# Kernel optimization log

Hardware: AMD Instinct MI355X
Metric: run time of the kernel (lower is better)

The kernel has to match this reference:

```python
import jax, jax.numpy as jnp
import numpy as np

B, N, IN, H, E = 8, 16383, 300, 512, 100  # complete binary tree, depth 14


def setup_inputs() -> dict:
    key = jax.random.key(0)
    ks = jax.random.split(key, 12)
    s = 0.05  # weight scale for numerical sanity
    return {
        "inputs": jax.random.normal(ks[0], (B, N, IN), jnp.float32),
        "edge_inputs": jax.random.normal(ks[1], (B, N, E), jnp.float32),
        "Wioux": jax.random.normal(ks[2], (3 * H, IN), jnp.float32) * s,
        "bioux": jax.random.normal(ks[3], (3 * H,), jnp.float32) * s,
        "Wiouh": jax.random.normal(ks[4], (3 * H, H), jnp.float32) * s,
        "biouh": jax.random.normal(ks[5], (3 * H,), jnp.float32) * s,
        "Wfx": jax.random.normal(ks[6], (H, IN), jnp.float32) * s,
        "bfx": jax.random.normal(ks[7], (H,), jnp.float32) * s,
        "Wfh": jax.random.normal(ks[8], (H, H), jnp.float32) * s,
        "bfh": jax.random.normal(ks[9], (H,), jnp.float32) * s,
        "We": jax.random.normal(ks[10], (H, E), jnp.float32) * s,
        "be": jax.random.normal(ks[11], (H,), jnp.float32) * s,
    }


def reference(inputs, edge_inputs, Wioux, bioux, Wiouh, biouh, Wfx, bfx, Wfh, bfh, We, be):
    # Level-batched TreeLSTM over a complete binary tree (BFS numbering:
    # children of node k are 2k+1, 2k+2). Same per-node math as the torch
    # recursion, with all nodes at a depth processed in one fused step.
    b, n_nodes, _ = inputs.shape
    hdim = Wiouh.shape[1]
    depth = int(np.log2(n_nodes + 1))
    h = jnp.zeros((b, n_nodes, hdim), inputs.dtype)
    c = jnp.zeros((b, n_nodes, hdim), inputs.dtype)
    for lvl in reversed(range(depth)):
        start = 2 ** lvl - 1
        n = 2 ** lvl
        x = inputs[:, start:start + n]                       # (B, n, IN)
        iou = jnp.einsum('bni,oi->bno', x, Wioux) + bioux + biouh
        if lvl == depth - 1:
            # leaves: child_c = child_h = 0, child_w = 0 => edge/f terms vanish
            fc_sum = jnp.zeros((b, n, hdim), inputs.dtype)
        else:
            cs = 2 * start + 1                               # first child index
            hc = h[:, cs:cs + 2 * n].reshape(b, n, 2, hdim)  # (B, n, 2, H)
            cc = c[:, cs:cs + 2 * n].reshape(b, n, 2, hdim)
            wc = edge_inputs[:, cs:cs + 2 * n].reshape(b, n, 2, -1)
            ex = jax.nn.sigmoid(jnp.einsum('bnke,he->bnkh', wc, We) + be)
            h_sum = (ex * hc).sum(axis=2)                    # edge-gated child sum
            iou = iou + jnp.einsum('bnh,oh->bno', h_sum, Wiouh)
            f = jax.nn.sigmoid(
                jnp.einsum('bnkh,oh->bnko', hc, Wfh) + bfh
                + (jnp.einsum('bni,hi->bnh', x, Wfx) + bfx)[:, :, None, :])
            fc_sum = (f * cc).sum(axis=2)
        i, o, u = jnp.split(iou, 3, axis=-1)
        c_lvl = jax.nn.sigmoid(i) * jnp.tanh(u) + fc_sum
        h_lvl = jax.nn.sigmoid(o) * jnp.tanh(c_lvl)
        c = c.at[:, start:start + n].set(c_lvl)
        h = h.at[:, start:start + n].set(h_lvl)
    # root state (c, h), concatenated along feature dim: (B, 2H)
    return jnp.concatenate([c[:, 0], h[:, 0]], axis=-1)
```

## Files before the change

kernel.cpp:

```cpp
#include <hip/hip_runtime.h>
#include <hip/hip_bf16.h>
#include <stdint.h>

#define B 8
#define NN 16383
#define INDIM 300
#define HDIM 512
#define EDIM 100

typedef short bf16x8 __attribute__((ext_vector_type(8)));
typedef float f32x4 __attribute__((ext_vector_type(4)));
typedef unsigned short ushort_t;

__device__ __forceinline__ float sigmoidf_(float v) { return 1.0f / (1.0f + __expf(-v)); }

__device__ __forceinline__ ushort_t f2b(float f) {
    union { float f; unsigned int u; } x; x.f = f;
    unsigned int u = x.u;
    return (ushort_t)((u + 0x7FFFu + ((u >> 16) & 1u)) >> 16);
}
__device__ __forceinline__ float b2f(ushort_t s) {
    union { float f; unsigned int u; } x; x.u = ((unsigned int)s) << 16; return x.f;
}
__device__ __forceinline__ bf16x8 zero8() {
    bf16x8 v;
#pragma unroll
    for (int i = 0; i < 8; ++i) v[i] = 0;
    return v;
}

__device__ __forceinline__ unsigned int pidx(int R, int col) {
    return (unsigned int)((R >> 4) * 8192 + (col >> 5) * 512 + ((col >> 3) & 3) * 128
                          + (R & 15) * 8 + (col & 7));
}

__device__ __forceinline__ size_t xlvl_base(int start) {
    return start ? (size_t)(start + 1) * 2560 : (size_t)0;
}

__global__ __launch_bounds__(256) void pack_kernel(
    const float* __restrict__ W, ushort_t* __restrict__ out,
    int Kdim, int Kt, int total)
{
    int idx = blockIdx.x * 256 + threadIdx.x;
    if (idx >= total) return;
    int lane = idx & 63;
    int kt = (idx >> 6) % Kt;
    int nt = idx / (Kt << 6);
    int n = nt * 16 + (lane & 15);
    int kb = kt * 32 + (lane >> 4) * 8;
    ushort_t v[8];
#pragma unroll
    for (int i = 0; i < 8; ++i) {
        int k = kb + i;
        v[i] = (k < Kdim) ? f2b(W[(size_t)n * Kdim + k]) : (ushort_t)0;
    }
    *reinterpret_cast<uint4*>(out + (size_t)idx * 8) = *reinterpret_cast<const uint4*>(v);
}

__global__ __launch_bounds__(256) void xpack_kernel(
    const float* __restrict__ inputs, ushort_t* __restrict__ xpk)
{
    int tid = blockIdx.x * 256 + threadIdx.x;
    if (tid >= NN * 8 * 40) return;
    int kr = tid & 3;
    int kt = (tid >> 2) % 10;
    int rb = tid / 40;
    int g = rb >> 3, b = rb & 7;
    int lvl = 31 - __clz(g + 1);
    int start = (1 << lvl) - 1;
    int R = (g - start) * 8 + b;
    int k0 = kt * 32 + kr * 8;
    ushort_t v[8];
#pragma unroll
    for (int i = 0; i < 8; i += 4) {
        int k = k0 + i;
        float4 xv = make_float4(0.f, 0.f, 0.f, 0.f);
        if (k + 4 <= INDIM)
            xv = *reinterpret_cast<const float4*>(&inputs[((size_t)b * NN + g) * INDIM + k]);
        v[i] = f2b(xv.x); v[i + 1] = f2b(xv.y); v[i + 2] = f2b(xv.z); v[i + 3] = f2b(xv.w);
    }
    size_t o = xlvl_base(start) + (size_t)(R >> 4) * 5120
             + (size_t)kt * 512 + (size_t)kr * 128 + (size_t)(R & 15) * 8;
    *reinterpret_cast<uint4*>(xpk + o) = *reinterpret_cast<const uint4*>(v);
}

__global__ __launch_bounds__(256) void children_kernel(
    const ushort_t* __restrict__ xpk, const float* __restrict__ edge_inputs,
    const ushort_t* __restrict__ pWfx, const float* __restrict__ bfx,
    const ushort_t* __restrict__ pWfh, const float* __restrict__ bfh,
    const ushort_t* __restrict__ pWe,  const float* __restrict__ be,
    const ushort_t* __restrict__ hX, const ushort_t* __restrict__ cX,
    ushort_t* __restrict__ hY, ushort_t* __restrict__ cY,
    int start, int n)
{
    const int nb = blockIdx.x * 4;
    const int pp = blockIdx.y;
    const int t = threadIdx.x;
    const int w = t >> 6, lane = t & 63;
    const int kr = lane >> 4, cl = lane & 15;

    __shared__ ushort_t wc[64][136];
    __shared__ ushort_t epi[64][264];

    for (int i = t; i < 64 * 32; i += 256) {
        int r = i >> 5, ch = i & 31;
        int kid = r >> 5, pr = r & 31, p = pr >> 3, b = pr & 7;
        int e = ch * 4;
        ushort_t vv[4] = {0, 0, 0, 0};
        if (e < EDIM && (nb + p) < n) {
            float4 xv = *reinterpret_cast<const float4*>(
                &edge_inputs[((size_t)b * NN + 2 * (start + nb + p) + 1 + kid) * EDIM + e]);
            vv[0] = f2b(xv.x); vv[1] = f2b(xv.y); vv[2] = f2b(xv.z); vv[3] = f2b(xv.w);
        }
        *reinterpret_cast<uint2*>(&wc[r][e]) = *reinterpret_cast<const uint2*>(vv);
    }
    __syncthreads();

    const bf16x8* fWfx = reinterpret_cast<const bf16x8*>(pWfx);
    const bf16x8* fWfh = reinterpret_cast<const bf16x8*>(pWfh);
    const bf16x8* fWe  = reinterpret_cast<const bf16x8*>(pWe);

    const ushort_t* xb = xpk + xlvl_base(start) + (size_t)(blockIdx.x * 2) * 5120 + (size_t)cl * 8;

    unsigned int cbase[4];
#pragma unroll
    for (int mt = 0; mt < 4; ++mt) {
        int kid = mt >> 1, mh = mt & 1;
        int p = 2 * mh + (cl >> 3);
        int b = cl & 7;
        cbase[mt] = ((nb + p) < n)
            ? (unsigned int)((nb + p) * 8192 + (kr * 16 + 8 * kid + b) * 8)
            : 0u;
    }

    const int ntb = w * 8 + pp * 4;

    f32x4 xfa[4][2];
#pragma unroll
    for (int q = 0; q < 4; ++q)
#pragma unroll
        for (int mh = 0; mh < 2; ++mh)
#pragma unroll
            for (int r = 0; r < 4; ++r) xfa[q][mh][r] = 0.f;
#pragma unroll 2
    for (int kt = 0; kt < 10; ++kt) {
        bf16x8 a0 = *reinterpret_cast<const bf16x8*>(xb + kt * 512 + kr * 128);
        bf16x8 a1 = *reinterpret_cast<const bf16x8*>(xb + 5120 + kt * 512 + kr * 128);
#pragma unroll
        for (int q = 0; q < 4; ++q) {
            bf16x8 bf_ = fWfx[(size_t)((ntb + q) * 10 + kt) * 64 + lane];
            xfa[q][0] = __builtin_amdgcn_mfma_f32_16x16x32_bf16(a0, bf_, xfa[q][0], 0, 0, 0);
            xfa[q][1] = __builtin_amdgcn_mfma_f32_16x16x32_bf16(a1, bf_, xfa[q][1], 0, 0, 0);
        }
    }
#pragma unroll
    for (int q = 0; q < 4; ++q) {
        float bv = bfx[(ntb + q) * 16 + cl];
#pragma unroll
        for (int mh = 0; mh < 2; ++mh)
#pragma unroll
            for (int r = 0; r < 4; ++r) xfa[q][mh][r] += bv;
    }

    {
        f32x4 eacc[4][4];
#pragma unroll
        for (int q = 0; q < 4; ++q)
#pragma unroll
            for (int mt = 0; mt < 4; ++mt)
#pragma unroll
                for (int r = 0; r < 4; ++r) eacc[q][mt][r] = 0.f;
#pragma unroll
        for (int kt = 0; kt < 4; ++kt) {
            bf16x8 av[4];
#pragma unroll
            for (int mt = 0; mt < 4; ++mt)
                av[mt] = *reinterpret_cast<const bf16x8*>(&wc[mt * 16 + cl][kt * 32 + kr * 8]);
#pragma unroll
            for (int q = 0; q < 4; ++q) {
                bf16x8 bf_ = fWe[(size_t)((ntb + q) * 4 + kt) * 64 + lane];
#pragma unroll
                for (int mt = 0; mt < 4; ++mt)
                    eacc[q][mt] = __builtin_amdgcn_mfma_f32_16x16x32_bf16(av[mt], bf_, eacc[q][mt], 0, 0, 0);
            }
        }
#pragma unroll
        for (int q = 0; q < 4; ++q) {
            float bev = be[(ntb + q) * 16 + cl];
#pragma unroll
            for (int mt = 0; mt < 4; ++mt)
#pragma unroll
                for (int r = 0; r < 4; ++r)
                    epi[mt * 16 + kr * 4 + r][(w * 4 + q) * 16 + cl] =
                        f2b(sigmoidf_(eacc[q][mt][r] + bev));
        }
    }
    __syncthreads();

#pragma unroll 1
    for (int it = 0; it < 4; ++it) {
        int task = it * 256 + t;
        int pb = task >> 5, cb = task & 31;
        int p = pb >> 3, b = pb & 7;
        if (nb + p < n) {
            int lc0 = cb * 8;
            int nt = ((cb >> 3) << 3) + pp * 4 + ((cb >> 1) & 3);
            int hh = cb & 1;
            int colc = (nt >> 1) * 512 + (((nt & 1) << 1) + hh) * 128;
            bf16x8 e0 = *reinterpret_cast<const bf16x8*>(&epi[pb][lc0]);
            bf16x8 e1 = *reinterpret_cast<const bf16x8*>(&epi[32 + pb][lc0]);
            const ushort_t* hb = hX + (unsigned int)((nb + p) * 8192 + colc + b * 8);
            bf16x8 h0 = *reinterpret_cast<const bf16x8*>(hb);
            bf16x8 h1 = *reinterpret_cast<const bf16x8*>(hb + 64);
            ushort_t res[8];
#pragma unroll
            for (int i = 0; i < 8; ++i)
                res[i] = f2b(b2f((ushort_t)e0[i]) * b2f((ushort_t)h0[i])
                           + b2f((ushort_t)e1[i]) * b2f((ushort_t)h1[i]));
            *reinterpret_cast<uint4*>(hY + (unsigned int)(((nb + p) >> 1) * 8192 + colc
                    + ((((nb + p) & 1) << 3) + b) * 8)) = *reinterpret_cast<const uint4*>(res);
        }
    }
    __syncthreads();

    {
        f32x4 facc[4][4];
#pragma unroll
        for (int q = 0; q < 4; ++q)
#pragma unroll
            for (int mt = 0; mt < 4; ++mt)
#pragma unroll
                for (int r = 0; r < 4; ++r) facc[q][mt][r] = 0.f;
#pragma unroll 4
        for (int kt = 0; kt < 16; ++kt) {
            bf16x8 av[4];
#pragma unroll
            for (int mt = 0; mt < 4; ++mt)
                av[mt] = *reinterpret_cast<const bf16x8*>(hX + cbase[mt] + kt * 512u);
#pragma unroll
            for (int q = 0; q < 4; ++q) {
                bf16x8 bf_ = fWfh[(size_t)((ntb + q) * 16 + kt) * 64 + lane];
#pragma unroll
                for (int mt = 0; mt < 4; ++mt)
                    facc[q][mt] = __builtin_amdgcn_mfma_f32_16x16x32_bf16(av[mt], bf_, facc[q][mt], 0, 0, 0);
            }
        }
#pragma unroll
        for (int q = 0; q < 4; ++q) {
            float bfhv = bfh[(ntb + q) * 16 + cl];
#pragma unroll
            for (int mt = 0; mt < 4; ++mt)
#pragma unroll
                for (int r = 0; r < 4; ++r)
                    epi[mt * 16 + kr * 4 + r][(w * 4 + q) * 16 + cl] =
                        f2b(sigmoidf_(facc[q][mt][r] + bfhv + xfa[q][mt & 1][r]));
        }
    }
    __syncthreads();

#pragma unroll 1
    for (int it = 0; it < 4; ++it) {
        int task = it * 256 + t;
        int pb = task >> 5, cb = task & 31;
        int p = pb >> 3, b = pb & 7;
        if (nb + p < n) {
            int lc0 = cb * 8;
            int nt = ((cb >> 3) << 3) + pp * 4 + ((cb >> 1) & 3);
            int hh = cb & 1;
            int colc = (nt >> 1) * 512 + (((nt & 1) << 1) + hh) * 128;
            bf16x8 f0 = *reinterpret_cast<const bf16x8*>(&epi[pb][lc0]);
            bf16x8 f1 = *reinterpret_cast<const bf16x8*>(&epi[32 + pb][lc0]);
            const ushort_t* cb_ = cX + (unsigned int)((nb + p) * 8192 + colc + b * 8);
            bf16x8 c0 = *reinterpret_cast<const bf16x8*>(cb_);
            bf16x8 c1 = *reinterpret_cast<const bf16x8*>(cb_ + 64);
            ushort_t res[8];
#pragma unroll
            for (int i = 0; i < 8; ++i)
                res[i] = f2b(b2f((ushort_t)f0[i]) * b2f((ushort_t)c0[i])
                           + b2f((ushort_t)f1[i]) * b2f((ushort_t)c1[i]));
            *reinterpret_cast<uint4*>(cY + (unsigned int)(((nb + p) >> 1) * 8192 + colc
                    + ((((nb + p) & 1) << 3) + b) * 8)) = *reinterpret_cast<const uint4*>(res);
        }
    }
}

template <bool LEAF, int JSPAN>
__global__ __launch_bounds__(256) void iou_kernel(
    const ushort_t* __restrict__ xpk,
    const ushort_t* __restrict__ pWioux, const float* __restrict__ bioux,
    const ushort_t* __restrict__ pWiouh, const float* __restrict__ biouh,
    const ushort_t* __restrict__ hYsum, const ushort_t* __restrict__ cYfc,
    ushort_t* __restrict__ hOut, ushort_t* __restrict__ cOut,
    int start, int n)
{
    const int nb = blockIdx.x * 8;
    const int t = threadIdx.x;
    const int w = t >> 6, lane = t & 63;
    const int kr = lane >> 4, cl = lane & 15;

    __shared__ ushort_t xsl[4 * 5120];
    __shared__ ushort_t p1[64][72];
    __shared__ ushort_t p2[64][72];

    {
        const ushort_t* xsrc = xpk + xlvl_base(start) + (size_t)(blockIdx.x * 4) * 5120;
        for (int i = t; i < 2560; i += 256)
            *reinterpret_cast<uint4*>(xsl + (size_t)i * 8) =
                *reinterpret_cast<const uint4*>(xsrc + (size_t)i * 8);
    }
    __syncthreads();

    const bf16x8* fWx = reinterpret_cast<const bf16x8*>(pWioux);
    const bf16x8* fWh = reinterpret_cast<const bf16x8*>(pWiouh);

    unsigned int hbase[4];
#pragma unroll
    for (int mt = 0; mt < 4; ++mt)
        hbase[mt] = (unsigned int)(((nb >> 1) + mt) * 8192 + lane * 8);

#pragma unroll 1
    for (int jj = 0; jj < JSPAN; ++jj) {
        const int j = blockIdx.y * JSPAN + jj;
        const int cnt = j * 4 + w;
        f32x4 acc[4][3];
#pragma unroll
        for (int mt = 0; mt < 4; ++mt)
#pragma unroll
            for (int q = 0; q < 3; ++q)
#pragma unroll
                for (int r = 0; r < 4; ++r) acc[mt][q][r] = 0.f;

#pragma unroll 2
        for (int kt = 0; kt < 10; ++kt) {
            bf16x8 av[4];
#pragma unroll
            for (int mt = 0; mt < 4; ++mt)
                av[mt] = *reinterpret_cast<const bf16x8*>(
                    xsl + mt * 5120 + kt * 512 + kr * 128 + cl * 8);
#pragma unroll
            for (int q = 0; q < 3; ++q) {
                bf16x8 bf_ = fWx[(size_t)((q * 32 + cnt) * 10 + kt) * 64 + lane];
#pragma unroll
                for (int mt = 0; mt < 4; ++mt)
                    acc[mt][q] = __builtin_amdgcn_mfma_f32_16x16x32_bf16(av[mt], bf_, acc[mt][q], 0, 0, 0);
            }
        }
        if (!LEAF) {
#pragma unroll 4
            for (int kt = 0; kt < 16; ++kt) {
                bf16x8 av[4];
#pragma unroll
                for (int mt = 0; mt < 4; ++mt)
                    av[mt] = *reinterpret_cast<const bf16x8*>(hYsum + hbase[mt] + kt * 512u);
#pragma unroll
                for (int q = 0; q < 3; ++q) {
                    bf16x8 bf_ = fWh[(size_t)((q * 32 + cnt) * 16 + kt) * 64 + lane];
#pragma unroll
                    for (int mt = 0; mt < 4; ++mt)
                        acc[mt][q] = __builtin_amdgcn_mfma_f32_16x16x32_bf16(av[mt], bf_, acc[mt][q], 0, 0, 0);
                }
            }
        }

        const int col = cnt * 16 + cl;
        const float bi = bioux[col]        + biouh[col];
        const float bo = bioux[col + 512]  + biouh[col + 512];
        const float bu = bioux[col + 1024] + biouh[col + 1024];
#pragma unroll
        for (int mt = 0; mt < 4; ++mt) {
#pragma unroll
            for (int r = 0; r < 4; ++r) {
                int row = mt * 16 + kr * 4 + r;
                float iv = acc[mt][0][r] + bi;
                float ov = acc[mt][1][r] + bo;
                float uv = acc[mt][2][r] + bu;
                p1[row][w * 16 + cl] = f2b(sigmoidf_(iv) * tanhf(uv));
                p2[row][w * 16 + cl] = f2b(sigmoidf_(ov));
            }
        }
        __syncthreads();

#pragma unroll 1
        for (int it = 0; it < 2; ++it) {
            int task = it * 256 + t;
            int rowid = task >> 3, ch = task & 7;
            int p = rowid >> 3, b = rowid & 7;
            if (nb + p < n) {
                int lc0 = ch * 8;
                int c2 = j * 4 + (ch >> 1);
                int hh = ch & 1;
                int colc = (c2 >> 1) * 512 + (((c2 & 1) << 1) + hh) * 128;
                unsigned int o = (unsigned int)(((nb + p) >> 1) * 8192 + colc
                                                + ((((nb + p) & 1) << 3) + b) * 8);
                bf16x8 v1 = *reinterpret_cast<const bf16x8*>(&p1[rowid][lc0]);
                bf16x8 v2 = *reinterpret_cast<const bf16x8*>(&p2[rowid][lc0]);
                bf16x8 vf = zero8();
                if (!LEAF) vf = *reinterpret_cast<const bf16x8*>(cYfc + o);
                ushort_t rh[8], rc[8];
#pragma unroll
                for (int i = 0; i < 8; ++i) {
                    float cv = b2f((ushort_t)v1[i]) + b2f((ushort_t)vf[i]);
                    float hv = b2f((ushort_t)v2[i]) * tanhf(cv);
                    rc[i] = f2b(cv); rh[i] = f2b(hv);
                }
                *reinterpret_cast<uint4*>(cOut + o) = *reinterpret_cast<const uint4*>(rc);
                *reinterpret_cast<uint4*>(hOut + o) = *reinterpret_cast<const uint4*>(rh);
            }
        }
        __syncthreads();
    }
}

__global__ __launch_bounds__(256) void out_kernel(
    const ushort_t* __restrict__ hroot, const ushort_t* __restrict__ croot,
    float* __restrict__ out)
{
    int t = blockIdx.x * 256 + threadIdx.x;
    if (t >= B * 2 * HDIM) return;
    int b = t / (2 * HDIM);
    int j = t - b * 2 * HDIM;
    int col = (j < HDIM) ? j : j - HDIM;
    unsigned int o = pidx(b, col);
    out[t] = (j < HDIM) ? b2f(croot[o]) : b2f(hroot[o]);
}

__global__ void diag_kernel(float* out, float v) { out[0] = v; }

extern "C" void kernel_launch(void* const* d_in, const int* in_sizes, int n_in,
                              void* d_out, int out_size, void* d_ws, size_t ws_size,
                              hipStream_t stream)
{
    const float* inputs      = (const float*)d_in[0];
    const float* edge_inputs = (const float*)d_in[1];
    const float* Wioux       = (const float*)d_in[2];
    const float* bioux       = (const float*)d_in[3];
    const float* Wiouh       = (const float*)d_in[4];
    const float* biouh       = (const float*)d_in[5];
    const float* Wfx         = (const float*)d_in[6];
    const float* bfx         = (const float*)d_in[7];
    const float* Wfh         = (const float*)d_in[8];
    const float* bfh         = (const float*)d_in[9];
    const float* We          = (const float*)d_in[10];
    const float* be          = (const float*)d_in[11];
    float* out = (float*)d_out;

    const size_t szWioux = (size_t)96 * 10 * 64 * 8;
    const size_t szWfx   = (size_t)32 * 10 * 64 * 8;
    const size_t szWe    = (size_t)32 * 4  * 64 * 8;
    const size_t szWfh   = (size_t)32 * 16 * 64 * 8;
    const size_t szWiouh = (size_t)96 * 16 * 64 * 8;

    const size_t eXpk = (size_t)16384 * 2560;
    const size_t eX   = (size_t)B * 8192 * HDIM;
    const size_t eY   = (size_t)B * 4096 * HDIM;

    const size_t need = (szWioux + szWfx + szWe + szWfh + szWiouh
                         + eXpk + 2 * eX + 2 * eY) * sizeof(ushort_t);
    if (ws_size < need) {
        diag_kernel<<<1, 1, 0, stream>>>(out, 2.0e8f);
        return;
    }

    ushort_t* p = (ushort_t*)d_ws;
    ushort_t* pWioux = p;            p += szWioux;
    ushort_t* pWfx   = p;            p += szWfx;
    ushort_t* pWe    = p;            p += szWe;
    ushort_t* pWfh   = p;            p += szWfh;
    ushort_t* pWiouh = p;            p += szWiouh;
    ushort_t* xpk = p;               p += eXpk;
    ushort_t* hX = p;                p += eX;
    ushort_t* cX = p;                p += eX;
    ushort_t* hY = p;                p += eY;
    ushort_t* cY = p;                p += eY;

    pack_kernel<<<(96 * 10 * 64 + 255) / 256, 256, 0, stream>>>(Wioux, pWioux, INDIM, 10, 96 * 10 * 64);
    pack_kernel<<<(32 * 10 * 64 + 255) / 256, 256, 0, stream>>>(Wfx,   pWfx,   INDIM, 10, 32 * 10 * 64);
    pack_kernel<<<(32 * 4  * 64 + 255) / 256, 256, 0, stream>>>(We,    pWe,    EDIM,  4,  32 * 4  * 64);
    pack_kernel<<<(32 * 16 * 64 + 255) / 256, 256, 0, stream>>>(Wfh,   pWfh,   HDIM,  16, 32 * 16 * 64);
    pack_kernel<<<(96 * 16 * 64 + 255) / 256, 256, 0, stream>>>(Wiouh, pWiouh, HDIM,  16, 96 * 16 * 64);
    xpack_kernel<<<(NN * 8 * 40 + 255) / 256, 256, 0, stream>>>(inputs, xpk);

    iou_kernel<true, 8><<<dim3(1024, 1), 256, 0, stream>>>(
        xpk, pWioux, bioux, pWiouh, biouh, hY, cY, hX, cX, 8191, 8192);

    for (int lvl = 12; lvl >= 0; --lvl) {
        int start = (1 << lvl) - 1;
        int n = 1 << lvl;
        children_kernel<<<dim3((n + 3) / 4, 2), 256, 0, stream>>>(
            xpk, edge_inputs, pWfx, bfx, pWfh, bfh, pWe, be,
            hX, cX, hY, cY, start, n);
        if (n >= 2048) {
            iou_kernel<false, 8><<<dim3(n / 8, 1), 256, 0, stream>>>(
                xpk, pWioux, bioux, pWiouh, biouh, hY, cY, hX, cX, start, n);
        } else {
            iou_kernel<false, 1><<<dim3((n + 7) / 8, 8), 256, 0, stream>>>(
                xpk, pWioux, bioux, pWiouh, biouh, hY, cY, hX, cX, start, n);
        }
    }

    out_kernel<<<(B * 2 * HDIM + 255) / 256, 256, 0, stream>>>(hX, cX, out);
}
```

Measured before the change: 1.473 ms.

## Swap MFMA operands to fuse gating epilogues directly from registers

Swaps the A/B operands of every MFMA so that each lane's accumulator holds four consecutive hidden columns for one row. This lets the edge-gate, forget-gate and node-update epilogues read child h/c, compute, and write packed outputs straight from registers. The shared-memory staging buffers (epi, p1, p2) and their __syncthreads round-trips are removed, which cuts LDS traffic and sync stalls and may improve occupancy. In exchange, global loads and stores shrink from 16-byte to 8-byte vectors, and sigmoid is recomputed per element instead of being stored once as bf16.

```diff
diff --git a/kernel.cpp b/kernel.cpp
--- a/kernel.cpp
+++ b/kernel.cpp
@@ -21,12 +21,6 @@
 }
 __device__ __forceinline__ float b2f(ushort_t s) {
     union { float f; unsigned int u; } x; x.u = ((unsigned int)s) << 16; return x.f;
-}
-__device__ __forceinline__ bf16x8 zero8() {
-    bf16x8 v;
-#pragma unroll
-    for (int i = 0; i < 8; ++i) v[i] = 0;
-    return v;
 }
 
 __device__ __forceinline__ unsigned int pidx(int R, int col) {
@@ -101,7 +95,6 @@
     const int kr = lane >> 4, cl = lane & 15;
 
     __shared__ ushort_t wc[64][136];
-    __shared__ ushort_t epi[64][264];
 
     for (int i = t; i < 64 * 32; i += 256) {
         int r = i >> 5, ch = i & 31;
@@ -135,6 +128,7 @@
     }
 
     const int ntb = w * 8 + pp * 4;
+    const int eo = (kr & 1) * 4;
 
     f32x4 xfa[4][2];
 #pragma unroll
@@ -150,17 +144,18 @@
 #pragma unroll
         for (int q = 0; q < 4; ++q) {
             bf16x8 bf_ = fWfx[(size_t)((ntb + q) * 10 + kt) * 64 + lane];
-            xfa[q][0] = __builtin_amdgcn_mfma_f32_16x16x32_bf16(a0, bf_, xfa[q][0], 0, 0, 0);
-            xfa[q][1] = __builtin_amdgcn_mfma_f32_16x16x32_bf16(a1, bf_, xfa[q][1], 0, 0, 0);
+            xfa[q][0] = __builtin_amdgcn_mfma_f32_16x16x32_bf16(bf_, a0, xfa[q][0], 0, 0, 0);
+            xfa[q][1] = __builtin_amdgcn_mfma_f32_16x16x32_bf16(bf_, a1, xfa[q][1], 0, 0, 0);
         }
     }
 #pragma unroll
     for (int q = 0; q < 4; ++q) {
-        float bv = bfx[(ntb + q) * 16 + cl];
+        float bv[4];
+        *reinterpret_cast<float4*>(bv) = *reinterpret_cast<const float4*>(&bfx[(ntb + q) * 16 + kr * 4]);
 #pragma unroll
         for (int mh = 0; mh < 2; ++mh)
 #pragma unroll
-            for (int r = 0; r < 4; ++r) xfa[q][mh][r] += bv;
+            for (int r = 0; r < 4; ++r) xfa[q][mh][r] += bv[r];
     }
 
     {
@@ -182,47 +177,37 @@
                 bf16x8 bf_ = fWe[(size_t)((ntb + q) * 4 + kt) * 64 + lane];
 #pragma unroll
                 for (int mt = 0; mt < 4; ++mt)
-                    eacc[q][mt] = __builtin_amdgcn_mfma_f32_16x16x32_bf16(av[mt], bf_, eacc[q][mt], 0, 0, 0);
+                    eacc[q][mt] = __builtin_amdgcn_mfma_f32_16x16x32_bf16(bf_, av[mt], eacc[q][mt], 0, 0, 0);
             }
         }
 #pragma unroll
         for (int q = 0; q < 4; ++q) {
-            float bev = be[(ntb + q) * 16 + cl];
-#pragma unroll
-            for (int mt = 0; mt < 4; ++mt)
-#pragma unroll
-                for (int r = 0; r < 4; ++r)
-                    epi[mt * 16 + kr * 4 + r][(w * 4 + q) * 16 + cl] =
-                        f2b(sigmoidf_(eacc[q][mt][r] + bev));
-        }
-    }
-    __syncthreads();
-
-#pragma unroll 1
-    for (int it = 0; it < 4; ++it) {
-        int task = it * 256 + t;
-        int pb = task >> 5, cb = task & 31;
-        int p = pb >> 3, b = pb & 7;
-        if (nb + p < n) {
-            int lc0 = cb * 8;
-            int nt = ((cb >> 3) << 3) + pp * 4 + ((cb >> 1) & 3);
-            int hh = cb & 1;
-            int colc = (nt >> 1) * 512 + (((nt & 1) << 1) + hh) * 128;
-            bf16x8 e0 = *reinterpret_cast<const bf16x8*>(&epi[pb][lc0]);
-            bf16x8 e1 = *reinterpret_cast<const bf16x8*>(&epi[32 + pb][lc0]);
-            const ushort_t* hb = hX + (unsigned int)((nb + p) * 8192 + colc + b * 8);
-            bf16x8 h0 = *reinterpret_cast<const bf16x8*>(hb);
-            bf16x8 h1 = *reinterpret_cast<const bf16x8*>(hb + 64);
-            ushort_t res[8];
-#pragma unroll
-            for (int i = 0; i < 8; ++i)
-                res[i] = f2b(b2f((ushort_t)e0[i]) * b2f((ushort_t)h0[i])
-                           + b2f((ushort_t)e1[i]) * b2f((ushort_t)h1[i]));
-            *reinterpret_cast<uint4*>(hY + (unsigned int)(((nb + p) >> 1) * 8192 + colc
-                    + ((((nb + p) & 1) << 3) + b) * 8)) = *reinterpret_cast<const uint4*>(res);
-        }
-    }
-    __syncthreads();
+            const int ct = ntb + q;
+            float be4[4];
+            *reinterpret_cast<float4*>(be4) = *reinterpret_cast<const float4*>(&be[ct * 16 + kr * 4]);
+            const int colc = (ct >> 1) * 512 + (((ct & 1) << 1) + (kr >> 1)) * 128;
+#pragma unroll
+            for (int mh = 0; mh < 2; ++mh) {
+                int pr = mh * 16 + cl;
+                int p = pr >> 3, b = pr & 7;
+                int np = nb + p;
+                if (np >= n) continue;
+                unsigned int hb0 = (unsigned int)(np * 8192 + colc + b * 8 + eo);
+                ushort_t h0s[4], h1s[4];
+                *reinterpret_cast<uint2*>(h0s) = *reinterpret_cast<const uint2*>(hX + hb0);
+                *reinterpret_cast<uint2*>(h1s) = *reinterpret_cast<const uint2*>(hX + hb0 + 64);
+                ushort_t res[4];
+#pragma unroll
+                for (int r = 0; r < 4; ++r) {
+                    float e0 = sigmoidf_(eacc[q][mh][r] + be4[r]);
+                    float e1 = sigmoidf_(eacc[q][mh + 2][r] + be4[r]);
+                    res[r] = f2b(e0 * b2f(h0s[r]) + e1 * b2f(h1s[r]));
+                }
+                *reinterpret_cast<uint2*>(hY + (unsigned int)((np >> 1) * 8192 + colc
+                        + (((np & 1) << 3) + b) * 8 + eo)) = *reinterpret_cast<const uint2*>(res);
+            }
+        }
+    }
 
     {
         f32x4 facc[4][4];
@@ -243,44 +228,36 @@
                 bf16x8 bf_ = fWfh[(size_t)((ntb + q) * 16 + kt) * 64 + lane];
 #pragma unroll
                 for (int mt = 0; mt < 4; ++mt)
-                    facc[q][mt] = __builtin_amdgcn_mfma_f32_16x16x32_bf16(av[mt], bf_, facc[q][mt], 0, 0, 0);
+                    facc[q][mt] = __builtin_amdgcn_mfma_f32_16x16x32_bf16(bf_, av[mt], facc[q][mt], 0, 0, 0);
             }
         }
 #pragma unroll
         for (int q = 0; q < 4; ++q) {
-            float bfhv = bfh[(ntb + q) * 16 + cl];
-#pragma unroll
-            for (int mt = 0; mt < 4; ++mt)
-#pragma unroll
-                for (int r = 0; r < 4; ++r)
-                    epi[mt * 16 + kr * 4 + r][(w * 4 + q) * 16 + cl] =
-                        f2b(sigmoidf_(facc[q][mt][r] + bfhv + xfa[q][mt & 1][r]));
-        }
-    }
-    __syncthreads();
-
-#pragma unroll 1
-    for (int it = 0; it < 4; ++it) {
-        int task = it * 256 + t;
-        int pb = task >> 5, cb = task & 31;
-        int p = pb >> 3, b = pb & 7;
-        if (nb + p < n) {
-            int lc0 = cb * 8;
-            int nt = ((cb >> 3) << 3) + pp * 4 + ((cb >> 1) & 3);
-            int hh = cb & 1;
-            int colc = (nt >> 1) * 512 + (((nt & 1) << 1) + hh) * 128;
-            bf16x8 f0 = *reinterpret_cast<const bf16x8*>(&epi[pb][lc0]);
-            bf16x8 f1 = *reinterpret_cast<const bf16x8*>(&epi[32 + pb][lc0]);
-            const ushort_t* cb_ = cX + (unsigned int)((nb + p) * 8192 + colc + b * 8);
-            bf16x8 c0 = *reinterpret_cast<const bf16x8*>(cb_);
-            bf16x8 c1 = *reinterpret_cast<const bf16x8*>(cb_ + 64);
-            ushort_t res[8];
-#pragma unroll
-            for (int i = 0; i < 8; ++i)
-                res[i] = f2b(b2f((ushort_t)f0[i]) * b2f((ushort_t)c0[i])
-                           + b2f((ushort_t)f1[i]) * b2f((ushort_t)c1[i]));
-            *reinterpret_cast<uint4*>(cY + (unsigned int)(((nb + p) >> 1) * 8192 + colc
-                    + ((((nb + p) & 1) << 3) + b) * 8)) = *reinterpret_cast<const uint4*>(res);
+            const int ct = ntb + q;
+            float bf4[4];
+            *reinterpret_cast<float4*>(bf4) = *reinterpret_cast<const float4*>(&bfh[ct * 16 + kr * 4]);
+            const int colc = (ct >> 1) * 512 + (((ct & 1) << 1) + (kr >> 1)) * 128;
+#pragma unroll
+            for (int mh = 0; mh < 2; ++mh) {
+                int pr = mh * 16 + cl;
+                int p = pr >> 3, b = pr & 7;
+                int np = nb + p;
+                if (np >= n) continue;
+                unsigned int cb0 = (unsigned int)(np * 8192 + colc + b * 8 + eo);
+                ushort_t c0s[4], c1s[4];
+                *reinterpret_cast<uint2*>(c0s) = *reinterpret_cast<const uint2*>(cX + cb0);
+                *reinterpret_cast<uint2*>(c1s) = *reinterpret_cast<const uint2*>(cX + cb0 + 64);
+                ushort_t res[4];
+#pragma unroll
+                for (int r = 0; r < 4; ++r) {
+                    float xfv = xfa[q][mh][r];
+                    float f0 = sigmoidf_(facc[q][mh][r] + bf4[r] + xfv);
+                    float f1 = sigmoidf_(facc[q][mh + 2][r] + bf4[r] + xfv);
+                    res[r] = f2b(f0 * b2f(c0s[r]) + f1 * b2f(c1s[r]));
+                }
+                *reinterpret_cast<uint2*>(cY + (unsigned int)((np >> 1) * 8192 + colc
+                        + (((np & 1) << 3) + b) * 8 + eo)) = *reinterpret_cast<const uint2*>(res);
+            }
         }
     }
 }
@@ -300,8 +277,6 @@
     const int kr = lane >> 4, cl = lane & 15;
 
     __shared__ ushort_t xsl[4 * 5120];
-    __shared__ ushort_t p1[64][72];
-    __shared__ ushort_t p2[64][72];
 
     {
         const ushort_t* xsrc = xpk + xlvl_base(start) + (size_t)(blockIdx.x * 4) * 5120;
@@ -319,6 +294,8 @@
     for (int mt = 0; mt < 4; ++mt)
         hbase[mt] = (unsigned int)(((nb >> 1) + mt) * 8192 + lane * 8);
 
+    const int eo = (kr & 1) * 4;
+
 #pragma unroll 1
     for (int jj = 0; jj < JSPAN; ++jj) {
         const int j = blockIdx.y * JSPAN + jj;
@@ -343,7 +320,7 @@
                 bf16x8 bf_ = fWx[(size_t)((q * 32 + cnt) * 10 + kt) * 64 + lane];
 #pragma unroll
                 for (int mt = 0; mt < 4; ++mt)
-                    acc[mt][q] = __builtin_amdgcn_mfma_f32_16x16x32_bf16(av[mt], bf_, acc[mt][q], 0, 0, 0);
+                    acc[mt][q] = __builtin_amdgcn_mfma_f32_16x16x32_bf16(bf_, av[mt], acc[mt][q], 0, 0, 0);
             }
         }
         if (!LEAF) {
@@ -358,57 +335,52 @@
                     bf16x8 bf_ = fWh[(size_t)((q * 32 + cnt) * 16 + kt) * 64 + lane];
 #pragma unroll
                     for (int mt = 0; mt < 4; ++mt)
-                        acc[mt][q] = __builtin_amdgcn_mfma_f32_16x16x32_bf16(av[mt], bf_, acc[mt][q], 0, 0, 0);
+                        acc[mt][q] = __builtin_amdgcn_mfma_f32_16x16x32_bf16(bf_, av[mt], acc[mt][q], 0, 0, 0);
                 }
             }
         }
 
-        const int col = cnt * 16 + cl;
-        const float bi = bioux[col]        + biouh[col];
-        const float bo = bioux[col + 512]  + biouh[col + 512];
-        const float bu = bioux[col + 1024] + biouh[col + 1024];
+        const int nbase = cnt * 16 + kr * 4;
+        float bi[4], bo[4], bu[4];
+        {
+            float x0[4], h0[4];
+            *reinterpret_cast<float4*>(x0) = *reinterpret_cast<const float4*>(&bioux[nbase]);
+            *reinterpret_cast<float4*>(h0) = *reinterpret_cast<const float4*>(&biouh[nbase]);
+#pragma unroll
+            for (int r = 0; r < 4; ++r) bi[r] = x0[r] + h0[r];
+            *reinterpret_cast<float4*>(x0) = *reinterpret_cast<const float4*>(&bioux[nbase + 512]);
+            *reinterpret_cast<float4*>(h0) = *reinterpret_cast<const float4*>(&biouh[nbase + 512]);
+#pragma unroll
+            for (int r = 0; r < 4; ++r) bo[r] = x0[r] + h0[r];
+            *reinterpret_cast<float4*>(x0) = *reinterpret_cast<const float4*>(&bioux[nbase + 1024]);
+            *reinterpret_cast<float4*>(h0) = *reinterpret_cast<const float4*>(&biouh[nbase + 1024]);
+#pragma unroll
+            for (int r = 0; r < 4; ++r) bu[r] = x0[r] + h0[r];
+        }
+        const int colc = (cnt >> 1) * 512 + (((cnt & 1) << 1) + (kr >> 1)) * 128;
 #pragma unroll
         for (int mt = 0; mt < 4; ++mt) {
+            int row = mt * 16 + cl;
+            int p = row >> 3, b = row & 7;
+            int np = nb + p;
+            if (np >= n) continue;
+            unsigned int off = (unsigned int)((np >> 1) * 8192 + colc
+                                              + (((np & 1) << 3) + b) * 8 + eo);
+            ushort_t fcs[4] = {0, 0, 0, 0};
+            if (!LEAF) *reinterpret_cast<uint2*>(fcs) = *reinterpret_cast<const uint2*>(cYfc + off);
+            ushort_t rc[4], rh[4];
 #pragma unroll
             for (int r = 0; r < 4; ++r) {
-                int row = mt * 16 + kr * 4 + r;
-                float iv = acc[mt][0][r] + bi;
-                float ov = acc[mt][1][r] + bo;
-                float uv = acc[mt][2][r] + bu;
-                p1[row][w * 16 + cl] = f2b(sigmoidf_(iv) * tanhf(uv));
-                p2[row][w * 16 + cl] = f2b(sigmoidf_(ov));
-            }
-        }
-        __syncthreads();
-
-#pragma unroll 1
-        for (int it = 0; it < 2; ++it) {
-            int task = it * 256 + t;
-            int rowid = task >> 3, ch = task & 7;
-            int p = rowid >> 3, b = rowid & 7;
-            if (nb + p < n) {
-                int lc0 = ch * 8;
-                int c2 = j * 4 + (ch >> 1);
-                int hh = ch & 1;
-                int colc = (c2 >> 1) * 512 + (((c2 & 1) << 1) + hh) * 128;
-                unsigned int o = (unsigned int)(((nb + p) >> 1) * 8192 + colc
-                                                + ((((nb + p) & 1) << 3) + b) * 8);
-                bf16x8 v1 = *reinterpret_cast<const bf16x8*>(&p1[rowid][lc0]);
-                bf16x8 v2 = *reinterpret_cast<const bf16x8*>(&p2[rowid][lc0]);
-                bf16x8 vf = zero8();
-                if (!LEAF) vf = *reinterpret_cast<const bf16x8*>(cYfc + o);
-                ushort_t rh[8], rc[8];
-#pragma unroll
-                for (int i = 0; i < 8; ++i) {
-                    float cv = b2f((ushort_t)v1[i]) + b2f((ushort_t)vf[i]);
-                    float hv = b2f((ushort_t)v2[i]) * tanhf(cv);
-                    rc[i] = f2b(cv); rh[i] = f2b(hv);
-                }
-                *reinterpret_cast<uint4*>(cOut + o) = *reinterpret_cast<const uint4*>(rc);
-                *reinterpret_cast<uint4*>(hOut + o) = *reinterpret_cast<const uint4*>(rh);
-            }
-        }
-        __syncthreads();
+                float iv = acc[mt][0][r] + bi[r];
+                float ov = acc[mt][1][r] + bo[r];
+                float uv = acc[mt][2][r] + bu[r];
+                float cv = sigmoidf_(iv) * tanhf(uv) + b2f(fcs[r]);
+                float hv = sigmoidf_(ov) * tanhf(cv);
+                rc[r] = f2b(cv); rh[r] = f2b(hv);
+            }
+            *reinterpret_cast<uint2*>(cOut + off) = *reinterpret_cast<const uint2*>(rc);
+            *reinterpret_cast<uint2*>(hOut + off) = *reinterpret_cast<const uint2*>(rh);
+        }
     }
 }
 
```

Measured after the change: 1.545 ms. 1.05x slower.
